# Optimization experiments

Hardware: AMD Instinct MI355X
Metric: run time of the kernel (lower is better)

The kernel has to match this reference:

```python
import jax, jax.numpy as jnp
import numpy as np

T = 2048        # packed token count (q_len)
HID = 2560      # hidden_size
H = 40          # num_heads
NOPE = 64       # qk_nope_head_dim
ROPE = 32       # qk_rope_head_dim
V = 64          # v_head_dim
QLORA = 768     # q_lora_rank
KVLORA = 256    # kv_lora_rank
EPS = 1e-5
THETA = 10000.0


def setup_inputs() -> dict:
    key = jax.random.key(0)
    ks = jax.random.split(key, 8)
    s = 0.02
    return {
        "positions": jnp.arange(T, dtype=jnp.int32),
        "hidden_states": jax.random.normal(ks[0], (T, HID), jnp.float32),
        "w_qa": jax.random.normal(ks[1], (HID, QLORA), jnp.float32) * s,
        "g_qa": jnp.ones((QLORA,), jnp.float32),
        "w_qb": jax.random.normal(ks[2], (QLORA, H * (NOPE + ROPE)), jnp.float32) * s,
        "w_kva": jax.random.normal(ks[3], (HID, KVLORA + ROPE), jnp.float32) * s,
        "g_kva": jnp.ones((KVLORA,), jnp.float32),
        "w_kc": jax.random.normal(ks[4], (H, NOPE, KVLORA), jnp.float32) * s,  # absorbed K weight
        "w_vc": jax.random.normal(ks[5], (H, KVLORA, V), jnp.float32) * s,     # absorbed V weight
        "w_o": jax.random.normal(ks[6], (H * V, HID), jnp.float32) * s,
    }


def _rms(x, g):
    return x * jax.lax.rsqrt(jnp.mean(x * x, axis=-1, keepdims=True) + EPS) * g


def _rope_rotate(x, cos, sin):
    # NeoX-style rotary: rotate halves of the last (ROPE) dim.
    half = ROPE // 2
    x1, x2 = x[..., :half], x[..., half:]
    return jnp.concatenate([x1 * cos - x2 * sin, x2 * cos + x1 * sin], axis=-1)


def reference(positions, hidden_states, w_qa, g_qa, w_qb, w_kva, g_kva, w_kc, w_vc, w_o):
    # Low-rank Q path: q_a_proj -> RMSNorm -> q_b_proj
    q = _rms(hidden_states @ w_qa, g_qa) @ w_qb                       # [T, H*(NOPE+ROPE)]
    q = q.reshape(T, H, NOPE + ROPE)
    q_nope, q_pe = q[..., :NOPE], q[..., NOPE:]

    # Weight absorption: project q_nope into latent space (bmm with w_kc)
    q_lat = jnp.einsum('thn,hnk->thk', q_nope, w_kc)                  # [T, H, KVLORA]

    # Compressed KV path (single shared latent head)
    latent = hidden_states @ w_kva                                    # [T, KVLORA+ROPE]
    v_in = _rms(latent[:, :KVLORA], g_kva)                            # [T, KVLORA]
    k_pe = latent[:, KVLORA:]                                         # [T, ROPE]

    # Partial-head RoPE on the rope slices
    half = ROPE // 2
    inv_freq = 1.0 / (THETA ** (jnp.arange(half, dtype=jnp.float32) / half))
    f = positions.astype(jnp.float32)[:, None] * inv_freq             # [T, half]
    cos, sin = jnp.cos(f), jnp.sin(f)
    q_pe = _rope_rotate(q_pe, cos[:, None, :], sin[:, None, :])       # [T, H, ROPE]
    k_pe = _rope_rotate(k_pe, cos, sin)                               # [T, ROPE]

    # Packed q/k feeding the latent-cache attention (MQA, head_dim = KVLORA+ROPE)
    q_in = jnp.concatenate([q_lat, q_pe], axis=-1)                    # [T, H, 288]
    k_in = jnp.concatenate([v_in, k_pe], axis=-1)                     # [T, 288]

    scale = (NOPE + ROPE) ** -0.5
    scores = jnp.einsum('thd,sd->hts', q_in, k_in) * scale            # [H, T, T]
    causal = jnp.tril(jnp.ones((T, T), dtype=bool))
    scores = jnp.where(causal, scores, -jnp.inf)
    probs = jax.nn.softmax(scores, axis=-1)
    o_lat = jnp.einsum('hts,sk->thk', probs, v_in)                    # [T, H, KVLORA]

    # Un-absorb: bmm with w_vc, then output projection
    o = jnp.einsum('thk,hkv->thv', o_lat, w_vc).reshape(T, H * V)     # [T, H*V]
    return o @ w_o                                                    # [T, HID]
```

## Files before the change

### kernel.cpp

```cpp
#include <hip/hip_runtime.h>
#include <hip/hip_bf16.h>
#include <math.h>

#define TT 2048
#define HID 2560
#define NH 40
#define NOPE 64
#define ROPE 32
#define VDIM 64
#define QLORA 768
#define KVLORA 256
#define DQK 288
#define QHD 96
#define EPS 1e-5f
#define THETA 10000.0f

typedef __attribute__((ext_vector_type(8))) short bf16x8;
typedef __attribute__((ext_vector_type(4))) float f32x4;
typedef __attribute__((address_space(1))) const void* gas_t;
typedef __attribute__((address_space(3))) void* las_t;

static __device__ __forceinline__ ushort f2bf(float x) {
    __hip_bfloat16 b = __float2bfloat16(x);
    return *reinterpret_cast<ushort*>(&b);
}

__global__ __launch_bounds__(256) void cast_bf16(const float* __restrict__ x,
                                                 ushort* __restrict__ y, int n) {
    int i = (blockIdx.x * 256 + threadIdx.x) * 4;
    if (i + 3 < n) {
        float4 v = *(const float4*)(x + i);
        y[i]     = f2bf(v.x);
        y[i + 1] = f2bf(v.y);
        y[i + 2] = f2bf(v.z);
        y[i + 3] = f2bf(v.w);
    }
}

__global__ __launch_bounds__(256) void transpose_cast(const float* __restrict__ w,
                                                      ushort* __restrict__ wt,
                                                      int K, int N) {
    __shared__ float tile[32][33];
    int bn = blockIdx.x * 32, bk = blockIdx.y * 32;
    int tx = threadIdx.x % 32, ty = threadIdx.x / 32;
    #pragma unroll
    for (int i = 0; i < 32; i += 8) {
        int k = bk + ty + i, n = bn + tx;
        if (k < K && n < N) tile[ty + i][tx] = w[(size_t)k * N + n];
    }
    __syncthreads();
    #pragma unroll
    for (int i = 0; i < 32; i += 8) {
        int n = bn + ty + i, k = bk + tx;
        if (n < N && k < K) wt[(size_t)n * K + k] = f2bf(tile[tx][ty + i]);
    }
}

__global__ __launch_bounds__(256, 2) void gemm_bf16(const ushort* __restrict__ A,
                                                    const ushort* __restrict__ Bt,
                                                    float* __restrict__ C,
                                                    int M, int N, int K) {
    __shared__ ushort As[128 * 32];
    __shared__ ushort Bs[128 * 32];
    const int tid  = threadIdx.x;
    const int lane = tid & 63;
    const int wv   = tid >> 6;
    const int col  = lane & 15;
    const int quad = lane >> 4;
    const int m0 = blockIdx.y * 128, n0 = blockIdx.x * 128;
    const int wr = (wv >> 1) * 64, wc = (wv & 1) * 64;

    f32x4 acc[4][4];
    #pragma unroll
    for (int i = 0; i < 4; i++)
        #pragma unroll
        for (int j = 0; j < 4; j++) acc[i][j] = (f32x4){0.f, 0.f, 0.f, 0.f};

    for (int k0 = 0; k0 < K; k0 += 32) {
        #pragma unroll
        for (int j = 0; j < 2; j++) {
            int slot = wv * 128 + j * 64 + lane;
            int row  = slot >> 2;
            int ch   = slot & 3;
            const ushort* ga = A + (size_t)(m0 + row) * K + k0 + ch * 8;
            __builtin_amdgcn_global_load_lds((gas_t)ga, (las_t)(As + slot * 8), 16, 0, 0);
            int brow = n0 + row; if (brow >= N) brow = N - 1;
            const ushort* gb = Bt + (size_t)brow * K + k0 + ch * 8;
            __builtin_amdgcn_global_load_lds((gas_t)gb, (las_t)(Bs + slot * 8), 16, 0, 0);
        }
        __syncthreads();
        bf16x8 af[4], bfr[4];
        #pragma unroll
        for (int i = 0; i < 4; i++)
            af[i] = *(const bf16x8*)(As + (wr + i * 16 + col) * 32 + quad * 8);
        #pragma unroll
        for (int j = 0; j < 4; j++)
            bfr[j] = *(const bf16x8*)(Bs + (wc + j * 16 + col) * 32 + quad * 8);
        #pragma unroll
        for (int i = 0; i < 4; i++)
            #pragma unroll
            for (int j = 0; j < 4; j++)
                acc[i][j] = __builtin_amdgcn_mfma_f32_16x16x32_bf16(af[i], bfr[j], acc[i][j], 0, 0, 0);
        __syncthreads();
    }
    #pragma unroll
    for (int i = 0; i < 4; i++) {
        int gr = m0 + wr + i * 16 + quad * 4;
        #pragma unroll
        for (int j = 0; j < 4; j++) {
            int gc = n0 + wc + j * 16 + col;
            if (gc < N) {
                #pragma unroll
                for (int r = 0; r < 4; r++)
                    C[(size_t)(gr + r) * N + gc] = acc[i][j][r];
            }
        }
    }
}

__global__ __launch_bounds__(256) void rms_qa(const float* __restrict__ x,
                                              const float* __restrict__ g,
                                              ushort* __restrict__ y) {
    int t = blockIdx.x, tid = threadIdx.x;
    __shared__ float red[256];
    __shared__ float s_inv;
    const float* row = x + (size_t)t * QLORA;
    float ss = 0.f;
    for (int i = tid; i < QLORA; i += 256) { float v = row[i]; ss += v * v; }
    red[tid] = ss; __syncthreads();
    for (int s = 128; s > 0; s >>= 1) { if (tid < s) red[tid] += red[tid + s]; __syncthreads(); }
    if (tid == 0) s_inv = rsqrtf(red[0] / (float)QLORA + EPS);
    __syncthreads();
    float si = s_inv;
    ushort* orow = y + (size_t)t * QLORA;
    for (int i = tid; i < QLORA; i += 256) orow[i] = f2bf(row[i] * si * g[i]);
}

__global__ __launch_bounds__(256) void kin_post(const float* __restrict__ kin,
                                                const float* __restrict__ g,
                                                const int* __restrict__ positions,
                                                ushort* __restrict__ kin_bf) {
    int t = blockIdx.x, tid = threadIdx.x;
    __shared__ float red[256];
    __shared__ float s_inv;
    const float* row = kin + (size_t)t * DQK;
    float v = row[tid];
    red[tid] = v * v; __syncthreads();
    for (int s = 128; s > 0; s >>= 1) { if (tid < s) red[tid] += red[tid + s]; __syncthreads(); }
    if (tid == 0) s_inv = rsqrtf(red[0] / (float)KVLORA + EPS);
    __syncthreads();
    ushort* orow = kin_bf + (size_t)t * DQK;
    orow[tid] = f2bf(v * s_inv * g[tid]);
    if (tid < 16) {
        float pos = (float)positions[t];
        float freq = powf(THETA, -(float)tid / 16.0f);
        float f = pos * freq;
        float c = cosf(f), s = sinf(f);
        float x1 = row[KVLORA + tid], x2 = row[KVLORA + 16 + tid];
        orow[KVLORA + tid]      = f2bf(x1 * c - x2 * s);
        orow[KVLORA + 16 + tid] = f2bf(x2 * c + x1 * s);
    }
}

#define QTB 16
__global__ __launch_bounds__(256) void build_qin(const float* __restrict__ q,
                                                 const float* __restrict__ w_kc,
                                                 const int* __restrict__ positions,
                                                 ushort* __restrict__ qin) {
    int tb = blockIdx.x * QTB, h = blockIdx.y, tid = threadIdx.x;
    const float scale = 0.10206207261596577f;
    __shared__ float qn[QTB][NOPE];
    __shared__ float qp[QTB][ROPE];
    for (int i = tid; i < QTB * QHD; i += 256) {
        int r = i / QHD, cidx = i % QHD;
        float v = q[(size_t)(tb + r) * (NH * QHD) + h * QHD + cidx];
        if (cidx < NOPE) qn[r][cidx] = v;
        else             qp[r][cidx - NOPE] = v;
    }
    __syncthreads();
    int k = tid;
    float acc[QTB];
    #pragma unroll
    for (int r = 0; r < QTB; r++) acc[r] = 0.f;
    const float* w = w_kc + (size_t)h * NOPE * KVLORA + k;
    for (int n = 0; n < NOPE; n++) {
        float wval = w[(size_t)n * KVLORA];
        #pragma unroll
        for (int r = 0; r < QTB; r++) acc[r] += qn[r][n] * wval;
    }
    #pragma unroll
    for (int r = 0; r < QTB; r++)
        qin[((size_t)(tb + r) * NH + h) * DQK + k] = f2bf(acc[r] * scale);
    int r = tid >> 4, fi = tid & 15;
    float pos = (float)positions[tb + r];
    float freq = powf(THETA, -(float)fi / 16.0f);
    float f = pos * freq;
    float c = cosf(f), s = sinf(f);
    float x1 = qp[r][fi], x2 = qp[r][16 + fi];
    ushort* orow = qin + ((size_t)(tb + r) * NH + h) * DQK;
    orow[KVLORA + fi]      = f2bf((x1 * c - x2 * s) * scale);
    orow[KVLORA + 16 + fi] = f2bf((x2 * c + x1 * s) * scale);
}

#define KVB 32
#define KSTR 296
#define VSTR 40
#define PSTR 40

__global__ __launch_bounds__(256, 3) void flash_attn(const ushort* __restrict__ qin,
                                                     const ushort* __restrict__ kin,
                                                     float* __restrict__ o_lat) {
    __shared__ __align__(16) ushort lds[KVB * KSTR + 256 * VSTR + 64 * PSTR];
    ushort* krow = lds;
    ushort* vt   = lds + KVB * KSTR;
    ushort* pbuf = vt + 256 * VSTR;

    const int tid  = threadIdx.x;
    const int lane = tid & 63;
    const int wv   = tid >> 6;
    const int col  = lane & 15;
    const int quad = lane >> 4;
    const int h    = blockIdx.y;
    const int qb   = ((int)gridDim.x - 1 - (int)blockIdx.x) * 64;

    const int srow = tid & 31;
    const int sgrp = tid >> 5;

    bf16x8 qf[9];
    {
        const ushort* base = qin + ((size_t)(qb + wv * 16 + col) * NH + h) * DQK + quad * 8;
        #pragma unroll
        for (int k = 0; k < 9; k++) qf[k] = *(const bf16x8*)(base + k * 32);
    }

    f32x4 of[16];
    #pragma unroll
    for (int i = 0; i < 16; i++) of[i] = (f32x4){0.f, 0.f, 0.f, 0.f};
    float m_i[4] = {-1e30f, -1e30f, -1e30f, -1e30f};
    float l_i[4] = {0.f, 0.f, 0.f, 0.f};

    const int rowg = qb + wv * 16 + quad * 4;

    for (int s0 = 0; s0 <= qb + 32; s0 += KVB) {
        __syncthreads();
        {
            const ushort* src = kin + (size_t)(s0 + srow) * DQK;
            #pragma unroll
            for (int ci = 0; ci < 4; ci++) {
                int c = ci * 8 + sgrp;
                uint4 u = *(const uint4*)(src + c * 8);
                *(uint4*)(krow + srow * KSTR + c * 8) = u;
                const ushort* up = (const ushort*)&u;
                #pragma unroll
                for (int j = 0; j < 8; j++)
                    vt[(c * 8 + j) * VSTR + srow] = up[j];
            }
            if (sgrp < 4) {
                int c = 32 + sgrp;
                uint4 u = *(const uint4*)(src + c * 8);
                *(uint4*)(krow + srow * KSTR + c * 8) = u;
            }
        }
        __syncthreads();

        f32x4 sf[2];
        sf[0] = (f32x4){0.f, 0.f, 0.f, 0.f};
        sf[1] = (f32x4){0.f, 0.f, 0.f, 0.f};
        __builtin_amdgcn_s_setprio(1);
        #pragma unroll
        for (int k = 0; k < 9; k++) {
            #pragma unroll
            for (int tc = 0; tc < 2; tc++) {
                bf16x8 bf = *(const bf16x8*)(krow + (tc * 16 + col) * KSTR + k * 32 + quad * 8);
                sf[tc] = __builtin_amdgcn_mfma_f32_16x16x32_bf16(qf[k], bf, sf[tc], 0, 0, 0);
            }
        }
        __builtin_amdgcn_s_setprio(0);

        #pragma unroll
        for (int tc = 0; tc < 2; tc++)
            #pragma unroll
            for (int r = 0; r < 4; r++)
                if (s0 + tc * 16 + col > rowg + r) sf[tc][r] = -1e30f;

        float mnew[4], alpha[4];
        #pragma unroll
        for (int r = 0; r < 4; r++) {
            float mx = fmaxf(sf[0][r], sf[1][r]);
            mx = fmaxf(mx, __shfl_xor(mx, 1));
            mx = fmaxf(mx, __shfl_xor(mx, 2));
            mx = fmaxf(mx, __shfl_xor(mx, 4));
            mx = fmaxf(mx, __shfl_xor(mx, 8));
            mnew[r] = fmaxf(m_i[r], mx);
            alpha[r] = __expf(m_i[r] - mnew[r]);
            m_i[r] = mnew[r];
        }
        float rsum[4];
        #pragma unroll
        for (int r = 0; r < 4; r++) {
            float s = 0.f;
            #pragma unroll
            for (int tc = 0; tc < 2; tc++) {
                float p = __expf(sf[tc][r] - mnew[r]);
                sf[tc][r] = p;
                s += p;
            }
            s += __shfl_xor(s, 1);
            s += __shfl_xor(s, 2);
            s += __shfl_xor(s, 4);
            s += __shfl_xor(s, 8);
            rsum[r] = s;
        }
        #pragma unroll
        for (int r = 0; r < 4; r++) l_i[r] = l_i[r] * alpha[r] + rsum[r];
        #pragma unroll
        for (int i = 0; i < 16; i++)
            #pragma unroll
            for (int r = 0; r < 4; r++) of[i][r] *= alpha[r];

        #pragma unroll
        for (int tc = 0; tc < 2; tc++)
            #pragma unroll
            for (int r = 0; r < 4; r++)
                pbuf[(wv * 16 + quad * 4 + r) * PSTR + tc * 16 + col] = f2bf(sf[tc][r]);
        bf16x8 pa = *(const bf16x8*)(pbuf + (wv * 16 + col) * PSTR + quad * 8);

        __builtin_amdgcn_s_setprio(1);
        #pragma unroll
        for (int nt = 0; nt < 16; nt++) {
            bf16x8 vb = *(const bf16x8*)(vt + (nt * 16 + col) * VSTR + quad * 8);
            of[nt] = __builtin_amdgcn_mfma_f32_16x16x32_bf16(pa, vb, of[nt], 0, 0, 0);
        }
        __builtin_amdgcn_s_setprio(0);
    }
    #pragma unroll
    for (int r = 0; r < 4; r++) {
        float inv = 1.0f / l_i[r];
        int row = qb + wv * 16 + quad * 4 + r;
        float* dst = o_lat + ((size_t)row * NH + h) * KVLORA + col;
        #pragma unroll
        for (int nt = 0; nt < 16; nt++) dst[nt * 16] = of[nt][r] * inv;
    }
}

__global__ __launch_bounds__(256) void ogemm(const float* __restrict__ o_lat,
                                             const float* __restrict__ w_vc,
                                             ushort* __restrict__ o) {
    int tb = blockIdx.x * 16, h = blockIdx.y, tid = threadIdx.x;
    __shared__ float ol[16][KVLORA];
    for (int i = tid; i < 16 * KVLORA; i += 256) {
        int r = i >> 8, k = i & 255;
        ol[r][k] = o_lat[((size_t)(tb + r) * NH + h) * KVLORA + k];
    }
    __syncthreads();
    int v = tid & 63, r0 = tid >> 6;
    float acc[4] = {0.f, 0.f, 0.f, 0.f};
    const float* w = w_vc + (size_t)h * KVLORA * VDIM + v;
    for (int k = 0; k < KVLORA; k++) {
        float wval = w[(size_t)k * VDIM];
        #pragma unroll
        for (int j = 0; j < 4; j++) acc[j] += ol[r0 + j * 4][k] * wval;
    }
    #pragma unroll
    for (int j = 0; j < 4; j++)
        o[(size_t)(tb + r0 + j * 4) * HID + h * VDIM + v] = f2bf(acc[j]);
}

extern "C" void kernel_launch(void* const* d_in, const int* in_sizes, int n_in,
                              void* d_out, int out_size, void* d_ws, size_t ws_size,
                              hipStream_t stream) {
    const int*   positions = (const int*)d_in[0];
    const float* hs    = (const float*)d_in[1];
    const float* w_qa  = (const float*)d_in[2];
    const float* g_qa  = (const float*)d_in[3];
    const float* w_qb  = (const float*)d_in[4];
    const float* w_kva = (const float*)d_in[5];
    const float* g_kva = (const float*)d_in[6];
    const float* w_kc  = (const float*)d_in[7];
    const float* w_vc  = (const float*)d_in[8];
    const float* w_o   = (const float*)d_in[9];
    float* out = (float*)d_out;

    float* ws    = (float*)d_ws;
    float* qa    = ws;
    float* q     = qa    + (size_t)TT * QLORA;
    float* kin   = q     + (size_t)TT * NH * QHD;
    float* o_lat = kin   + (size_t)TT * DQK;
    ushort* ub     = (ushort*)(o_lat + (size_t)TT * NH * KVLORA);
    ushort* hs_bf  = ub;
    ushort* qa_bf  = hs_bf  + (size_t)TT * HID;
    ushort* o_bf   = qa_bf  + (size_t)TT * QLORA;
    ushort* kin_bf = o_bf   + (size_t)TT * HID;
    ushort* qin_bf = kin_bf + (size_t)TT * DQK;
    ushort* w_qa_t  = qin_bf + (size_t)TT * NH * DQK;
    ushort* w_qb_t  = w_qa_t + (size_t)QLORA * HID;
    ushort* w_kva_t = w_qb_t + (size_t)(NH * QHD) * QLORA;
    ushort* w_o_t   = w_kva_t + (size_t)DQK * HID;

    cast_bf16<<<(TT * HID) / 1024, 256, 0, stream>>>(hs, hs_bf, TT * HID);
    transpose_cast<<<dim3(QLORA / 32, HID / 32), 256, 0, stream>>>(w_qa, w_qa_t, HID, QLORA);
    transpose_cast<<<dim3((NH * QHD) / 32, QLORA / 32), 256, 0, stream>>>(w_qb, w_qb_t, QLORA, NH * QHD);
    transpose_cast<<<dim3(DQK / 32, HID / 32), 256, 0, stream>>>(w_kva, w_kva_t, HID, DQK);
    transpose_cast<<<dim3(HID / 32, HID / 32), 256, 0, stream>>>(w_o, w_o_t, HID, HID);

    gemm_bf16<<<dim3(QLORA / 128, TT / 128), 256, 0, stream>>>(hs_bf, w_qa_t, qa, TT, QLORA, HID);
    rms_qa<<<TT, 256, 0, stream>>>(qa, g_qa, qa_bf);
    gemm_bf16<<<dim3((NH * QHD) / 128, TT / 128), 256, 0, stream>>>(qa_bf, w_qb_t, q, TT, NH * QHD, QLORA);
    gemm_bf16<<<dim3((DQK + 127) / 128, TT / 128), 256, 0, stream>>>(hs_bf, w_kva_t, kin, TT, DQK, HID);
    kin_post<<<TT, 256, 0, stream>>>(kin, g_kva, positions, kin_bf);
    build_qin<<<dim3(TT / QTB, NH), 256, 0, stream>>>(q, w_kc, positions, qin_bf);
    flash_attn<<<dim3(TT / 64, NH), 256, 0, stream>>>(qin_bf, kin_bf, o_lat);
    ogemm<<<dim3(TT / 16, NH), 256, 0, stream>>>(o_lat, w_vc, o_bf);
    gemm_bf16<<<dim3(HID / 128, TT / 128), 256, 0, stream>>>(o_bf, w_o_t, out, TT, HID, HID);
}
```

Measured before the change: 880.3 us.

## Process two heads per attention block to share K/V tiles; add N64 GEMM

The flash attention kernel now runs 512 threads covering two heads. Both heads share one LDS K/V tile, which halves the global loads and transposes per head, and each head keeps its own P buffer. A new 128x64-tile GEMM replaces the 128x128 GEMM for the q_a and kv_a projections to increase block count for their small N. The stricter launch bounds may raise register pressure or cause spills in the attention kernel.

```diff
diff --git a/kernel.cpp b/kernel.cpp
--- a/kernel.cpp
+++ b/kernel.cpp
@@ -109,6 +109,72 @@
         #pragma unroll
         for (int j = 0; j < 4; j++) {
             int gc = n0 + wc + j * 16 + col;
+            if (gc < N) {
+                #pragma unroll
+                for (int r = 0; r < 4; r++)
+                    C[(size_t)(gr + r) * N + gc] = acc[i][j][r];
+            }
+        }
+    }
+}
+
+__global__ __launch_bounds__(256, 4) void gemm_bf16_n64(const ushort* __restrict__ A,
+                                                        const ushort* __restrict__ Bt,
+                                                        float* __restrict__ C,
+                                                        int M, int N, int K) {
+    __shared__ ushort As[128 * 32];
+    __shared__ ushort Bs[64 * 32];
+    const int tid  = threadIdx.x;
+    const int lane = tid & 63;
+    const int wv   = tid >> 6;
+    const int col  = lane & 15;
+    const int quad = lane >> 4;
+    const int m0 = blockIdx.y * 128, n0 = blockIdx.x * 64;
+    const int wr = wv * 32;
+
+    f32x4 acc[2][4];
+    #pragma unroll
+    for (int i = 0; i < 2; i++)
+        #pragma unroll
+        for (int j = 0; j < 4; j++) acc[i][j] = (f32x4){0.f, 0.f, 0.f, 0.f};
+
+    for (int k0 = 0; k0 < K; k0 += 32) {
+        #pragma unroll
+        for (int j = 0; j < 2; j++) {
+            int slot = j * 256 + tid;
+            int row  = slot >> 2;
+            int ch   = slot & 3;
+            const ushort* ga = A + (size_t)(m0 + row) * K + k0 + ch * 8;
+            __builtin_amdgcn_global_load_lds((gas_t)ga, (las_t)(As + slot * 8), 16, 0, 0);
+        }
+        {
+            int row = tid >> 2;
+            int ch  = tid & 3;
+            int brow = n0 + row; if (brow >= N) brow = N - 1;
+            const ushort* gb = Bt + (size_t)brow * K + k0 + ch * 8;
+            __builtin_amdgcn_global_load_lds((gas_t)gb, (las_t)(Bs + tid * 8), 16, 0, 0);
+        }
+        __syncthreads();
+        bf16x8 af[2], bfr[4];
+        #pragma unroll
+        for (int i = 0; i < 2; i++)
+            af[i] = *(const bf16x8*)(As + (wr + i * 16 + col) * 32 + quad * 8);
+        #pragma unroll
+        for (int j = 0; j < 4; j++)
+            bfr[j] = *(const bf16x8*)(Bs + (j * 16 + col) * 32 + quad * 8);
+        #pragma unroll
+        for (int i = 0; i < 2; i++)
+            #pragma unroll
+            for (int j = 0; j < 4; j++)
+                acc[i][j] = __builtin_amdgcn_mfma_f32_16x16x32_bf16(af[i], bfr[j], acc[i][j], 0, 0, 0);
+        __syncthreads();
+    }
+    #pragma unroll
+    for (int i = 0; i < 2; i++) {
+        int gr = m0 + wr + i * 16 + quad * 4;
+        #pragma unroll
+        for (int j = 0; j < 4; j++) {
+            int gc = n0 + j * 16 + col;
             if (gc < N) {
                 #pragma unroll
                 for (int r = 0; r < 4; r++)
@@ -207,10 +273,10 @@
 #define VSTR 40
 #define PSTR 40
 
-__global__ __launch_bounds__(256, 3) void flash_attn(const ushort* __restrict__ qin,
+__global__ __launch_bounds__(512, 6) void flash_attn(const ushort* __restrict__ qin,
                                                      const ushort* __restrict__ kin,
                                                      float* __restrict__ o_lat) {
-    __shared__ __align__(16) ushort lds[KVB * KSTR + 256 * VSTR + 64 * PSTR];
+    __shared__ __align__(16) ushort lds[KVB * KSTR + 256 * VSTR + 2 * 64 * PSTR];
     ushort* krow = lds;
     ushort* vt   = lds + KVB * KSTR;
     ushort* pbuf = vt + 256 * VSTR;
@@ -218,17 +284,19 @@
     const int tid  = threadIdx.x;
     const int lane = tid & 63;
     const int wv   = tid >> 6;
+    const int wvq  = wv & 3;
     const int col  = lane & 15;
     const int quad = lane >> 4;
-    const int h    = blockIdx.y;
+    const int h    = blockIdx.y * 2 + (wv >> 2);
     const int qb   = ((int)gridDim.x - 1 - (int)blockIdx.x) * 64;
+    ushort* pb = pbuf + (wv >> 2) * 64 * PSTR;
 
     const int srow = tid & 31;
     const int sgrp = tid >> 5;
 
     bf16x8 qf[9];
     {
-        const ushort* base = qin + ((size_t)(qb + wv * 16 + col) * NH + h) * DQK + quad * 8;
+        const ushort* base = qin + ((size_t)(qb + wvq * 16 + col) * NH + h) * DQK + quad * 8;
         #pragma unroll
         for (int k = 0; k < 9; k++) qf[k] = *(const bf16x8*)(base + k * 32);
     }
@@ -239,15 +307,15 @@
     float m_i[4] = {-1e30f, -1e30f, -1e30f, -1e30f};
     float l_i[4] = {0.f, 0.f, 0.f, 0.f};
 
-    const int rowg = qb + wv * 16 + quad * 4;
+    const int rowg = qb + wvq * 16 + quad * 4;
 
     for (int s0 = 0; s0 <= qb + 32; s0 += KVB) {
         __syncthreads();
         {
             const ushort* src = kin + (size_t)(s0 + srow) * DQK;
             #pragma unroll
-            for (int ci = 0; ci < 4; ci++) {
-                int c = ci * 8 + sgrp;
+            for (int ci = 0; ci < 2; ci++) {
+                int c = ci * 16 + sgrp;
                 uint4 u = *(const uint4*)(src + c * 8);
                 *(uint4*)(krow + srow * KSTR + c * 8) = u;
                 const ushort* up = (const ushort*)&u;
@@ -322,8 +390,8 @@
         for (int tc = 0; tc < 2; tc++)
             #pragma unroll
             for (int r = 0; r < 4; r++)
-                pbuf[(wv * 16 + quad * 4 + r) * PSTR + tc * 16 + col] = f2bf(sf[tc][r]);
-        bf16x8 pa = *(const bf16x8*)(pbuf + (wv * 16 + col) * PSTR + quad * 8);
+                pb[(wvq * 16 + quad * 4 + r) * PSTR + tc * 16 + col] = f2bf(sf[tc][r]);
+        bf16x8 pa = *(const bf16x8*)(pb + (wvq * 16 + col) * PSTR + quad * 8);
 
         __builtin_amdgcn_s_setprio(1);
         #pragma unroll
@@ -336,7 +404,7 @@
     #pragma unroll
     for (int r = 0; r < 4; r++) {
         float inv = 1.0f / l_i[r];
-        int row = qb + wv * 16 + quad * 4 + r;
+        int row = qb + wvq * 16 + quad * 4 + r;
         float* dst = o_lat + ((size_t)row * NH + h) * KVLORA + col;
         #pragma unroll
         for (int nt = 0; nt < 16; nt++) dst[nt * 16] = of[nt][r] * inv;
@@ -403,13 +471,13 @@
     transpose_cast<<<dim3(DQK / 32, HID / 32), 256, 0, stream>>>(w_kva, w_kva_t, HID, DQK);
     transpose_cast<<<dim3(HID / 32, HID / 32), 256, 0, stream>>>(w_o, w_o_t, HID, HID);
 
-    gemm_bf16<<<dim3(QLORA / 128, TT / 128), 256, 0, stream>>>(hs_bf, w_qa_t, qa, TT, QLORA, HID);
+    gemm_bf16_n64<<<dim3(QLORA / 64, TT / 128), 256, 0, stream>>>(hs_bf, w_qa_t, qa, TT, QLORA, HID);
     rms_qa<<<TT, 256, 0, stream>>>(qa, g_qa, qa_bf);
     gemm_bf16<<<dim3((NH * QHD) / 128, TT / 128), 256, 0, stream>>>(qa_bf, w_qb_t, q, TT, NH * QHD, QLORA);
-    gemm_bf16<<<dim3((DQK + 127) / 128, TT / 128), 256, 0, stream>>>(hs_bf, w_kva_t, kin, TT, DQK, HID);
+    gemm_bf16_n64<<<dim3((DQK + 63) / 64, TT / 128), 256, 0, stream>>>(hs_bf, w_kva_t, kin, TT, DQK, HID);
     kin_post<<<TT, 256, 0, stream>>>(kin, g_kva, positions, kin_bf);
     build_qin<<<dim3(TT / QTB, NH), 256, 0, stream>>>(q, w_kc, positions, qin_bf);
-    flash_attn<<<dim3(TT / 64, NH), 256, 0, stream>>>(qin_bf, kin_bf, o_lat);
+    flash_attn<<<dim3(TT / 64, NH / 2), 512, 0, stream>>>(qin_bf, kin_bf, o_lat);
     ogemm<<<dim3(TT / 16, NH), 256, 0, stream>>>(o_lat, w_vc, o_bf);
     gemm_bf16<<<dim3(HID / 128, TT / 128), 256, 0, stream>>>(o_bf, w_o_t, out, TT, HID, HID);
 }
```

Measured after the change: 1.617 ms. 1.84x slower.
